# Optimization experiments

Hardware: AMD Instinct MI355X
Metric: run time of the kernel (lower is better)

Reference implementation:

```python
import jax, jax.numpy as jnp
import numpy as np

# 3x3 window roll offsets, row-major as in PatchShift2D.shift_content
SHIFTS = [(1, 1), (1, 0), (1, -1), (0, 1), (0, 0), (0, -1), (-1, 1), (-1, 0), (-1, -1)]
NUM_WIN = 9


def patch_shift(x, inv):
    # x: [B, T, H, W, C]; pad C up to multiple of 9 and H,W by 1, roll each
    # of the 9 channel groups by a distinct (h, w) offset, then crop back.
    B, T, H, W, C = x.shape
    Ch = int(np.ceil(C / NUM_WIN) * NUM_WIN)
    xp = jnp.pad(x, ((0, 0), (0, 0), (1, 1), (1, 1), (0, Ch - C)))
    m = -1 if inv else 1
    parts = jnp.split(xp, NUM_WIN, axis=-1)
    shifted = [jnp.roll(p, (m * sh, m * sw), axis=(2, 3))
               for p, (sh, sw) in zip(parts, SHIFTS)]
    return jnp.concatenate(shifted, axis=-1)[:, :, 1:H + 1, 1:W + 1, :C]


def _gelu(v):
    return jax.nn.gelu(v, approximate=False)  # torch nn.GELU default (erf)


def setup_inputs() -> dict:
    key = jax.random.key(0)
    ks = jax.random.split(key, 14)
    B, T, H, W, C = 2, 8, 56, 56, 512
    HID = 1024
    s = 0.02
    return {
        "x": jax.random.normal(ks[0], (B, T, H, W, C), dtype=jnp.float32),
        "fc_w": s * jax.random.normal(ks[1], (C, HID), dtype=jnp.float32),
        "fc_b": jnp.zeros((HID,), jnp.float32),
        "fc1_w": s * jax.random.normal(ks[2], (HID, C), dtype=jnp.float32),
        "fc1_b": jnp.zeros((C,), jnp.float32),
        "fc2_w": s * jax.random.normal(ks[3], (HID, C), dtype=jnp.float32),
        "fc2_b": jnp.zeros((C,), jnp.float32),
        "rw1_w": s * jax.random.normal(ks[4], (C, C // 4), dtype=jnp.float32),
        "rw1_b": jnp.zeros((C // 4,), jnp.float32),
        "rw2_w": s * jax.random.normal(ks[5], (C // 4, 2 * C), dtype=jnp.float32),
        "rw2_b": jnp.zeros((2 * C,), jnp.float32),
        "proj_w": s * jax.random.normal(ks[6], (C, C), dtype=jnp.float32),
        "proj_b": jnp.zeros((C,), jnp.float32),
    }


def reference(x, fc_w, fc_b, fc1_w, fc1_b, fc2_w, fc2_b,
              rw1_w, rw1_b, rw2_w, rw2_b, proj_w, proj_b):
    B, T, H, W, C = x.shape
    xh = _gelu(x @ fc_w + fc_b)                                  # [B,T,H,W,HID]
    h = patch_shift(_gelu(patch_shift(xh, False) @ fc1_w + fc1_b), True)  # [B,T,H,W,C]
    w = _gelu(xh @ fc2_w + fc2_b)                                 # [B,T,H,W,C]
    a = (h + w).mean(axis=(1, 2, 3))                              # [B,C]
    a = _gelu(a @ rw1_w + rw1_b) @ rw2_w + rw2_b                  # [B,2C]
    a = jax.nn.softmax(a.reshape(B, C, 2).transpose(2, 0, 1), axis=0)  # [2,B,C]
    a = a[:, :, None, None, None, :]                              # [2,B,1,1,1,C]
    out = h * a[0] + w * a[1]
    return out @ proj_w + proj_b
```

## Files before the change

### kernel.cpp

```cpp
#include <hip/hip_runtime.h>
#include <hip/hip_bf16.h>
#include <stdint.h>


typedef __attribute__((ext_vector_type(8))) short short8;
typedef __attribute__((ext_vector_type(4))) float floatx4;
typedef unsigned int uint;
typedef unsigned short ushort;

#define NTOK   50176
#define HWIMG  3136

__device__ __forceinline__ float gelu_exact(float v) {
    return 0.5f * v * (1.0f + erff(v * 0.70710678118654752440f));
}
__device__ __forceinline__ float gelu_fast(float v) {
    float u = v * (0.7978845608f + 0.0356774081f * v * v);
    return v * __builtin_amdgcn_rcpf(1.0f + __expf(-2.0f * u));
}

__device__ __forceinline__ int shift_h(int g) { return 1 - g / 3; }
__device__ __forceinline__ int shift_w(int g) { return 1 - g % 3; }

typedef const __attribute__((address_space(1))) uint* gas_ptr;
typedef __attribute__((address_space(3))) uint* las_ptr;

__device__ __forceinline__ void async_copy16(const void* g, void* l) {
    gas_ptr gp = (gas_ptr)(uintptr_t)g;
    las_ptr lp = (las_ptr)(uint32_t)(uintptr_t)l;
    __builtin_amdgcn_global_load_lds(gp, lp, 16, 0, 0);
}

template <int EPI>
__global__ __launch_bounds__(256) void gemm_bt(
    const __hip_bfloat16* __restrict__ A,
    const __hip_bfloat16* __restrict__ Bt,
    const float* __restrict__ bias,
    void* __restrict__ Cout, __hip_bfloat16* __restrict__ Cout2,
    float* __restrict__ ssum, int N, int K)
{
    __shared__ __hip_bfloat16 As[128 * 32];
    __shared__ __hip_bfloat16 Bs[128 * 32];

    const int t    = threadIdx.x;
    const int lane = t & 63;
    const int wave = t >> 6;
    const int wm   = wave >> 1;
    const int wn   = wave & 1;

    const int nbn  = gridDim.x;
    const int flat = blockIdx.y * nbn + blockIdx.x;
    const int xcd  = flat & 7;
    const int j    = flat >> 3;
    const int jd   = j / nbn;
    const int bm   = xcd * 49 + jd;
    const int bn   = j - jd * nbn;

    const __hip_bfloat16* ga0 = A  + (size_t)(bm * 128 + (t >> 2)) * K + (t & 3) * 8;
    const __hip_bfloat16* ga1 = ga0 + (size_t)64 * K;
    const __hip_bfloat16* gb0 = Bt + (size_t)(bn * 128 + (t >> 2)) * K + (t & 3) * 8;
    const __hip_bfloat16* gb1 = gb0 + (size_t)64 * K;
    __hip_bfloat16* la0 = &As[t * 8];
    __hip_bfloat16* la1 = &As[t * 8 + 2048];
    __hip_bfloat16* lb0 = &Bs[t * 8];
    __hip_bfloat16* lb1 = &Bs[t * 8 + 2048];

    floatx4 acc[4][4] = {};

    const int kq = (lane >> 4) * 8;
    const int ml = lane & 15;

    for (int k0 = 0; k0 < K; k0 += 32) {
        async_copy16(ga0, la0);
        async_copy16(ga1, la1);
        async_copy16(gb0, lb0);
        async_copy16(gb1, lb1);
        ga0 += 32; ga1 += 32; gb0 += 32; gb1 += 32;
        asm volatile("s_waitcnt vmcnt(0)" ::: "memory");
        __syncthreads();

        short8 af[4], bf[4];
#pragma unroll
        for (int i = 0; i < 4; i++) {
            af[i] = *(const short8*)&As[(wm * 64 + i * 16 + ml) * 32 + kq];
            bf[i] = *(const short8*)&Bs[(wn * 64 + i * 16 + ml) * 32 + kq];
        }
#pragma unroll
        for (int mi = 0; mi < 4; mi++)
#pragma unroll
            for (int ni = 0; ni < 4; ni++)
                acc[mi][ni] = __builtin_amdgcn_mfma_f32_16x16x32_bf16(
                    af[mi], bf[ni], acc[mi][ni], 0, 0, 0);
        __syncthreads();
    }

    const int rq = (lane >> 4) * 4;

    int cols[4], gsh[4], gsw[4];
    float bv[4];
    float sum[4] = {0.f, 0.f, 0.f, 0.f};
#pragma unroll
    for (int ni = 0; ni < 4; ni++) {
        const int col = bn * 128 + wn * 64 + ni * 16 + ml;
        cols[ni] = col;
        bv[ni] = bias[col];
        if (EPI == 1) { const int g = col / 114; gsh[ni] = shift_h(g); gsw[ni] = shift_w(g); }
        if (EPI == 2) { const int g = col / 57;  gsh[ni] = shift_h(g); gsw[ni] = shift_w(g); }
    }

#pragma unroll
    for (int mi = 0; mi < 4; mi++) {
        const int row0 = bm * 128 + wm * 64 + mi * 16 + rq;
        int phr[4], pwr[4];
        if (EPI == 1 || EPI == 2) {
            const int bt_ = row0 / HWIMG;
            const int rem = row0 - bt_ * HWIMG;
            const int ph0 = rem / 56;
            const int pw0 = rem - ph0 * 56;
#pragma unroll
            for (int r = 0; r < 4; r++) {
                int pw = pw0 + r, ph = ph0;
                if (pw >= 56) { pw -= 56; ph += 1; }
                if (ph >= 56) { ph = 0; }
                phr[r] = ph; pwr[r] = pw;
            }
        }
#pragma unroll
        for (int ni = 0; ni < 4; ni++) {
            const int col = cols[ni];
#pragma unroll
            for (int r = 0; r < 4; r++) {
                const int tok = row0 + r;
                float v = acc[mi][ni][r] + bv[ni];
                if (EPI != 0) v = gelu_fast(v);
                if (EPI == 0) {
                    ((float*)Cout)[(size_t)tok * N + col] = v;
                } else if (EPI == 1) {
                    const __hip_bfloat16 bvv = __float2bfloat16(v);
                    ((__hip_bfloat16*)Cout)[(size_t)tok * N + col] = bvv;
                    const int th = phr[r] + gsh[ni], tw = pwr[r] + gsw[ni];
                    if ((unsigned)th < 56u && (unsigned)tw < 56u)
                        Cout2[(size_t)(tok + gsh[ni] * 56 + gsw[ni]) * N + col] = bvv;
                } else if (EPI == 2) {
                    const int th = phr[r] - gsh[ni], tw = pwr[r] - gsw[ni];
                    if ((unsigned)th < 56u && (unsigned)tw < 56u) {
                        ((__hip_bfloat16*)Cout)[(size_t)(tok - gsh[ni] * 56 - gsw[ni]) * N + col]
                            = __float2bfloat16(v);
                        sum[ni] += v;
                    }
                } else {
                    ((__hip_bfloat16*)Cout)[(size_t)tok * N + col] = __float2bfloat16(v);
                    sum[ni] += v;
                }
            }
        }
    }

    if (EPI == 2 || EPI == 3) {
        const int b = (bm >= 196) ? 1 : 0;
#pragma unroll
        for (int ni = 0; ni < 4; ni++) {
            float s = sum[ni];
            s += __shfl_xor(s, 16, 64);
            s += __shfl_xor(s, 32, 64);
            if (lane < 16) atomicAdd(&ssum[b * 512 + cols[ni]], s);
        }
    }
}

template <int C, int GS, int SGN>
__global__ __launch_bounds__(256) void zero_holes(__hip_bfloat16* __restrict__ buf)
{
    const int i = blockIdx.x * 256 + threadIdx.x;
    const int c = i % C;
    const int p = i / C;
    const int bt = p / 220, fp = p % 220;
    int oh, ow;
    if (fp < 56)       { oh = 0;        ow = fp; }
    else if (fp < 112) { oh = 55;       ow = fp - 56; }
    else if (fp < 166) { oh = fp - 111; ow = 0; }
    else               { oh = fp - 165; ow = 55; }
    const int g = c / GS;
    const int ih = oh - SGN * shift_h(g);
    const int iw = ow - SGN * shift_w(g);
    if ((unsigned)ih >= 56u || (unsigned)iw >= 56u)
        buf[((size_t)(bt * HWIMG + oh * 56 + ow)) * C + c] = __float2bfloat16(0.0f);
}

__global__ __launch_bounds__(256) void cvt_x(const float4* __restrict__ x,
                                             __hip_bfloat16* __restrict__ xb)
{
    int i = blockIdx.x * 256 + threadIdx.x;
    float4 v = x[i];
    __hip_bfloat16 b0 = __float2bfloat16(v.x);
    __hip_bfloat16 b1 = __float2bfloat16(v.y);
    __hip_bfloat16 b2 = __float2bfloat16(v.z);
    __hip_bfloat16 b3 = __float2bfloat16(v.w);
    uint2 o;
    o.x = (uint)*(ushort*)&b0 | ((uint)*(ushort*)&b1 << 16);
    o.y = (uint)*(ushort*)&b2 | ((uint)*(ushort*)&b3 << 16);
    *(uint2*)&xb[(size_t)i * 4] = o;
}

__global__ __launch_bounds__(256) void prep_w(
    const float* __restrict__ fcw,  const float* __restrict__ fc1w,
    const float* __restrict__ fc2w, const float* __restrict__ projw,
    __hip_bfloat16* __restrict__ fcwT, __hip_bfloat16* __restrict__ fc1T,
    __hip_bfloat16* __restrict__ fc2T, __hip_bfloat16* __restrict__ projT)
{
    int i = blockIdx.x * 256 + threadIdx.x;
    if (i < 524288) {
        int n = i >> 9, k = i & 511;
        fcwT[i] = __float2bfloat16(fcw[k * 1024 + n]);
    } else if (i < 1048576) {
        int j = i - 524288;
        int n = j >> 10, k = j & 1023;
        fc1T[j] = __float2bfloat16(fc1w[k * 512 + n]);
    } else if (i < 1572864) {
        int j = i - 1048576;
        int n = j >> 10, k = j & 1023;
        fc2T[j] = __float2bfloat16(fc2w[k * 512 + n]);
    } else if (i < 1835008) {
        int j = i - 1572864;
        int n = j >> 9, k = j & 511;
        projT[j] = __float2bfloat16(projw[k * 512 + n]);
    }
}

__global__ __launch_bounds__(256) void tiny_mlp(
    const float* __restrict__ s0, const float* __restrict__ s1,
    const float* __restrict__ rw1_w, const float* __restrict__ rw1_b,
    const float* __restrict__ rw2_w, const float* __restrict__ rw2_b,
    float* __restrict__ a0, float* __restrict__ a1)
{
    __shared__ float mean[1024];
    __shared__ float z[256];
    __shared__ float av[2048];
    const int t = threadIdx.x;
    for (int i = t; i < 1024; i += 256)
        mean[i] = (s0[i] + s1[i]) * (1.0f / 25088.0f);
    __syncthreads();
    {
        const int b = t >> 7, j = t & 127;
        float acc = rw1_b[j];
        for (int cc = 0; cc < 512; cc++)
            acc += mean[b * 512 + cc] * rw1_w[cc * 128 + j];
        z[t] = gelu_exact(acc);
    }
    __syncthreads();
    for (int i = t; i < 2048; i += 256) {
        const int b = i >> 10, o = i & 1023;
        float acc = rw2_b[o];
        for (int j = 0; j < 128; j++)
            acc += z[b * 128 + j] * rw2_w[j * 1024 + o];
        av[i] = acc;
    }
    __syncthreads();
    for (int i = t; i < 1024; i += 256) {
        const int b = i >> 9, cc = i & 511;
        const float x0 = av[b * 1024 + 2 * cc];
        const float x1 = av[b * 1024 + 2 * cc + 1];
        const float m = fmaxf(x0, x1);
        const float e0 = expf(x0 - m), e1 = expf(x1 - m);
        const float inv = 1.0f / (e0 + e1);
        a0[i] = e0 * inv;
        a1[i] = e1 * inv;
    }
}

__device__ __forceinline__ float bf_lo(uint u) { return __uint_as_float(u << 16); }
__device__ __forceinline__ float bf_hi(uint u) { return __uint_as_float(u & 0xffff0000u); }
__device__ __forceinline__ uint pack_bf2(float lo, float hi) {
    __hip_bfloat16 a = __float2bfloat16(lo), b = __float2bfloat16(hi);
    return (uint)*(ushort*)&a | ((uint)*(ushort*)&b << 16);
}

__global__ __launch_bounds__(256) void combine(
    const uint4* __restrict__ hs4, const uint4* __restrict__ w4,
    const float* __restrict__ a0, const float* __restrict__ a1,
    uint4* __restrict__ hw4)
{
    const int i = blockIdx.x * 256 + threadIdx.x;
    const int ck = i & 63;
    const int tok = i >> 6;
    const int b = (tok >= 25088) ? 1 : 0;
    const float4* A0 = (const float4*)&a0[b * 512 + ck * 8];
    const float4* A1 = (const float4*)&a1[b * 512 + ck * 8];
    const float4 s0l = A0[0], s0h = A0[1];
    const float4 s1l = A1[0], s1h = A1[1];
    const uint4 h = hs4[i], w = w4[i];
    uint4 o;
    o.x = pack_bf2(bf_lo(h.x) * s0l.x + bf_lo(w.x) * s1l.x,
                   bf_hi(h.x) * s0l.y + bf_hi(w.x) * s1l.y);
    o.y = pack_bf2(bf_lo(h.y) * s0l.z + bf_lo(w.y) * s1l.z,
                   bf_hi(h.y) * s0l.w + bf_hi(w.y) * s1l.w);
    o.z = pack_bf2(bf_lo(h.z) * s0h.x + bf_lo(w.z) * s1h.x,
                   bf_hi(h.z) * s0h.y + bf_hi(w.z) * s1h.y);
    o.w = pack_bf2(bf_lo(h.w) * s0h.z + bf_lo(w.w) * s1h.z,
                   bf_hi(h.w) * s0h.w + bf_hi(w.w) * s1h.w);
    hw4[i] = o;
}

extern "C" void kernel_launch(void* const* d_in, const int* in_sizes, int n_in,
                              void* d_out, int out_size, void* d_ws, size_t ws_size,
                              hipStream_t stream)
{
    const float* x      = (const float*)d_in[0];
    const float* fc_w   = (const float*)d_in[1];
    const float* fc_b   = (const float*)d_in[2];
    const float* fc1_w  = (const float*)d_in[3];
    const float* fc1_b  = (const float*)d_in[4];
    const float* fc2_w  = (const float*)d_in[5];
    const float* fc2_b  = (const float*)d_in[6];
    const float* rw1_w  = (const float*)d_in[7];
    const float* rw1_b  = (const float*)d_in[8];
    const float* rw2_w  = (const float*)d_in[9];
    const float* rw2_b  = (const float*)d_in[10];
    const float* proj_w = (const float*)d_in[11];
    const float* proj_b = (const float*)d_in[12];

    uint8_t* ws = (uint8_t*)d_ws;
    __hip_bfloat16* xh  = (__hip_bfloat16*)(ws);
    __hip_bfloat16* xb  = (__hip_bfloat16*)(ws + 102760448);
    uint8_t* wt         = ws + 102760448 + 51380224;
    __hip_bfloat16* fcwT  = (__hip_bfloat16*)(wt);
    __hip_bfloat16* fc1T  = fcwT + 524288;
    __hip_bfloat16* fc2T  = fc1T + 524288;
    __hip_bfloat16* projT = fc2T + 524288;
    float* s0 = (float*)(wt + 3670016);
    float* s1 = s0 + 1024;
    float* a0 = s1 + 1024;
    float* a1 = a0 + 1024;

    __hip_bfloat16* xs   = (__hip_bfloat16*)d_out;
    __hip_bfloat16* wbuf = (__hip_bfloat16*)d_out;
    __hip_bfloat16* hs   = xb;
    __hip_bfloat16* hw   = xh;

    hipMemsetAsync(s0, 0, 8192, stream);

    zero_holes<1024, 114, +1><<<14080, 256, 0, stream>>>(xs);
    cvt_x<<<25088, 256, 0, stream>>>((const float4*)x, xb);
    prep_w<<<7168, 256, 0, stream>>>(fc_w, fc1_w, fc2_w, proj_w, fcwT, fc1T, fc2T, projT);

    gemm_bt<1><<<dim3(8, 392), 256, 0, stream>>>(xb, fcwT, fc_b, xh, xs, nullptr, 1024, 512);
    zero_holes<512, 57, -1><<<7040, 256, 0, stream>>>(hs);
    gemm_bt<2><<<dim3(4, 392), 256, 0, stream>>>(xs, fc1T, fc1_b, hs, nullptr, s0, 512, 1024);
    gemm_bt<3><<<dim3(4, 392), 256, 0, stream>>>(xh, fc2T, fc2_b, wbuf, nullptr, s1, 512, 1024);
    tiny_mlp<<<1, 256, 0, stream>>>(s0, s1, rw1_w, rw1_b, rw2_w, rw2_b, a0, a1);
    combine<<<12544, 256, 0, stream>>>((const uint4*)hs, (const uint4*)wbuf, a0, a1, (uint4*)hw);
    gemm_bt<0><<<dim3(4, 392), 256, 0, stream>>>(hw, projT, proj_b, d_out, nullptr, nullptr, 512, 512);
}
```

Baseline: 663.4 us.

## Double-buffer GEMM LDS tiles and transpose MFMA output for vectorized epilogue stores

```diff
diff --git a/kernel.cpp b/kernel.cpp
--- a/kernel.cpp
+++ b/kernel.cpp
@@ -21,6 +21,11 @@
 
 __device__ __forceinline__ int shift_h(int g) { return 1 - g / 3; }
 __device__ __forceinline__ int shift_w(int g) { return 1 - g % 3; }
+
+__device__ __forceinline__ uint pack_bf2(float lo, float hi) {
+    __hip_bfloat16 a = __float2bfloat16(lo), b = __float2bfloat16(hi);
+    return (uint)*(ushort*)&a | ((uint)*(ushort*)&b << 16);
+}
 
 typedef const __attribute__((address_space(1))) uint* gas_ptr;
 typedef __attribute__((address_space(3))) uint* las_ptr;
@@ -39,8 +44,8 @@
     void* __restrict__ Cout, __hip_bfloat16* __restrict__ Cout2,
     float* __restrict__ ssum, int N, int K)
 {
-    __shared__ __hip_bfloat16 As[128 * 32];
-    __shared__ __hip_bfloat16 Bs[128 * 32];
+    __shared__ __align__(16) __hip_bfloat16 As[2][128 * 32];
+    __shared__ __align__(16) __hip_bfloat16 Bs[2][128 * 32];
 
     const int t    = threadIdx.x;
     const int lane = t & 63;
@@ -60,97 +65,134 @@
     const __hip_bfloat16* ga1 = ga0 + (size_t)64 * K;
     const __hip_bfloat16* gb0 = Bt + (size_t)(bn * 128 + (t >> 2)) * K + (t & 3) * 8;
     const __hip_bfloat16* gb1 = gb0 + (size_t)64 * K;
-    __hip_bfloat16* la0 = &As[t * 8];
-    __hip_bfloat16* la1 = &As[t * 8 + 2048];
-    __hip_bfloat16* lb0 = &Bs[t * 8];
-    __hip_bfloat16* lb1 = &Bs[t * 8 + 2048];
+    const int t8 = t * 8;
 
     floatx4 acc[4][4] = {};
-
     const int kq = (lane >> 4) * 8;
     const int ml = lane & 15;
 
-    for (int k0 = 0; k0 < K; k0 += 32) {
-        async_copy16(ga0, la0);
-        async_copy16(ga1, la1);
-        async_copy16(gb0, lb0);
-        async_copy16(gb1, lb1);
+    auto stage = [&](int buf) {
+        async_copy16(ga0, &As[buf][t8]);
+        async_copy16(ga1, &As[buf][t8 + 2048]);
+        async_copy16(gb0, &Bs[buf][t8]);
+        async_copy16(gb1, &Bs[buf][t8 + 2048]);
         ga0 += 32; ga1 += 32; gb0 += 32; gb1 += 32;
-        asm volatile("s_waitcnt vmcnt(0)" ::: "memory");
-        __syncthreads();
+    };
+
+    const int nt = K >> 5;
+    stage(0);
+    __syncthreads();
+
+    for (int tt = 0; tt < nt; ++tt) {
+        const int cur = tt & 1;
+        if (tt + 1 < nt) stage(cur ^ 1);
 
         short8 af[4], bf[4];
 #pragma unroll
         for (int i = 0; i < 4; i++) {
-            af[i] = *(const short8*)&As[(wm * 64 + i * 16 + ml) * 32 + kq];
-            bf[i] = *(const short8*)&Bs[(wn * 64 + i * 16 + ml) * 32 + kq];
+            af[i] = *(const short8*)&As[cur][(wm * 64 + i * 16 + ml) * 32 + kq];
+            bf[i] = *(const short8*)&Bs[cur][(wn * 64 + i * 16 + ml) * 32 + kq];
         }
 #pragma unroll
         for (int mi = 0; mi < 4; mi++)
 #pragma unroll
             for (int ni = 0; ni < 4; ni++)
                 acc[mi][ni] = __builtin_amdgcn_mfma_f32_16x16x32_bf16(
-                    af[mi], bf[ni], acc[mi][ni], 0, 0, 0);
+                    bf[ni], af[mi], acc[mi][ni], 0, 0, 0);
+
         __syncthreads();
     }
 
-    const int rq = (lane >> 4) * 4;
-
-    int cols[4], gsh[4], gsw[4];
-    float bv[4];
-    float sum[4] = {0.f, 0.f, 0.f, 0.f};
+    const int rq  = (lane >> 4) * 4;
+    const int chb = bn * 128 + wn * 64 + rq;
+    const int tkb = bm * 128 + wm * 64 + ml;
+
+    float s_ac[4][4];
+    if (EPI == 2 || EPI == 3)
+#pragma unroll
+        for (int ni = 0; ni < 4; ni++)
+#pragma unroll
+            for (int r = 0; r < 4; r++) s_ac[ni][r] = 0.f;
+
 #pragma unroll
     for (int ni = 0; ni < 4; ni++) {
-        const int col = bn * 128 + wn * 64 + ni * 16 + ml;
-        cols[ni] = col;
-        bv[ni] = bias[col];
-        if (EPI == 1) { const int g = col / 114; gsh[ni] = shift_h(g); gsw[ni] = shift_w(g); }
-        if (EPI == 2) { const int g = col / 57;  gsh[ni] = shift_h(g); gsw[ni] = shift_w(g); }
-    }
-
-#pragma unroll
-    for (int mi = 0; mi < 4; mi++) {
-        const int row0 = bm * 128 + wm * 64 + mi * 16 + rq;
-        int phr[4], pwr[4];
+        const int ch0 = chb + ni * 16;
+        const float4 b4 = *(const float4*)&bias[ch0];
+        int gsh = 0, gsw = 0;
+        bool guni = true;
         if (EPI == 1 || EPI == 2) {
-            const int bt_ = row0 / HWIMG;
-            const int rem = row0 - bt_ * HWIMG;
-            const int ph0 = rem / 56;
-            const int pw0 = rem - ph0 * 56;
-#pragma unroll
-            for (int r = 0; r < 4; r++) {
-                int pw = pw0 + r, ph = ph0;
-                if (pw >= 56) { pw -= 56; ph += 1; }
-                if (ph >= 56) { ph = 0; }
-                phr[r] = ph; pwr[r] = pw;
+            const int DIV = (EPI == 1) ? 114 : 57;
+            const int g0 = ch0 / DIV, g3 = (ch0 + 3) / DIV;
+            guni = (g0 == g3);
+            gsh = shift_h(g0); gsw = shift_w(g0);
+        }
+#pragma unroll
+        for (int mi = 0; mi < 4; mi++) {
+            const int tok = tkb + mi * 16;
+            float v[4];
+            v[0] = acc[mi][ni][0] + b4.x;
+            v[1] = acc[mi][ni][1] + b4.y;
+            v[2] = acc[mi][ni][2] + b4.z;
+            v[3] = acc[mi][ni][3] + b4.w;
+            if (EPI != 0) {
+#pragma unroll
+                for (int r = 0; r < 4; r++) v[r] = gelu_fast(v[r]);
             }
-        }
-#pragma unroll
-        for (int ni = 0; ni < 4; ni++) {
-            const int col = cols[ni];
-#pragma unroll
-            for (int r = 0; r < 4; r++) {
-                const int tok = row0 + r;
-                float v = acc[mi][ni][r] + bv[ni];
-                if (EPI != 0) v = gelu_fast(v);
-                if (EPI == 0) {
-                    ((float*)Cout)[(size_t)tok * N + col] = v;
-                } else if (EPI == 1) {
-                    const __hip_bfloat16 bvv = __float2bfloat16(v);
-                    ((__hip_bfloat16*)Cout)[(size_t)tok * N + col] = bvv;
-                    const int th = phr[r] + gsh[ni], tw = pwr[r] + gsw[ni];
-                    if ((unsigned)th < 56u && (unsigned)tw < 56u)
-                        Cout2[(size_t)(tok + gsh[ni] * 56 + gsw[ni]) * N + col] = bvv;
-                } else if (EPI == 2) {
-                    const int th = phr[r] - gsh[ni], tw = pwr[r] - gsw[ni];
-                    if ((unsigned)th < 56u && (unsigned)tw < 56u) {
-                        ((__hip_bfloat16*)Cout)[(size_t)(tok - gsh[ni] * 56 - gsw[ni]) * N + col]
-                            = __float2bfloat16(v);
-                        sum[ni] += v;
+
+            if (EPI == 0) {
+                float4 o; o.x = v[0]; o.y = v[1]; o.z = v[2]; o.w = v[3];
+                *(float4*)&((float*)Cout)[(size_t)tok * N + ch0] = o;
+            } else {
+                uint2 u;
+                u.x = pack_bf2(v[0], v[1]);
+                u.y = pack_bf2(v[2], v[3]);
+
+                if (EPI == 1 || EPI == 3)
+                    *(uint2*)&((__hip_bfloat16*)Cout)[(size_t)tok * N + ch0] = u;
+
+                if (EPI == 1 || EPI == 2) {
+                    const int rem = tok - (tok / HWIMG) * HWIMG;
+                    const int ph = rem / 56, pw = rem - ph * 56;
+                    if (EPI == 1) {
+                        if (guni) {
+                            if ((unsigned)(ph + gsh) < 56u && (unsigned)(pw + gsw) < 56u)
+                                *(uint2*)&Cout2[(size_t)(tok + gsh * 56 + gsw) * N + ch0] = u;
+                        } else {
+#pragma unroll
+                            for (int r = 0; r < 4; r++) {
+                                const int g = (ch0 + r) / 114;
+                                const int sh = shift_h(g), sw = shift_w(g);
+                                if ((unsigned)(ph + sh) < 56u && (unsigned)(pw + sw) < 56u)
+                                    Cout2[(size_t)(tok + sh * 56 + sw) * N + ch0 + r]
+                                        = __float2bfloat16(v[r]);
+                            }
+                        }
+                    } else {
+                        if (guni) {
+                            if ((unsigned)(ph - gsh) < 56u && (unsigned)(pw - gsw) < 56u) {
+                                *(uint2*)&((__hip_bfloat16*)Cout)
+                                    [(size_t)(tok - gsh * 56 - gsw) * N + ch0] = u;
+#pragma unroll
+                                for (int r = 0; r < 4; r++) s_ac[ni][r] += v[r];
+                            }
+                        } else {
+#pragma unroll
+                            for (int r = 0; r < 4; r++) {
+                                const int g = (ch0 + r) / 57;
+                                const int sh = shift_h(g), sw = shift_w(g);
+                                if ((unsigned)(ph - sh) < 56u && (unsigned)(pw - sw) < 56u) {
+                                    ((__hip_bfloat16*)Cout)
+                                        [(size_t)(tok - sh * 56 - sw) * N + ch0 + r]
+                                        = __float2bfloat16(v[r]);
+                                    s_ac[ni][r] += v[r];
+                                }
+                            }
+                        }
                     }
-                } else {
-                    ((__hip_bfloat16*)Cout)[(size_t)tok * N + col] = __float2bfloat16(v);
-                    sum[ni] += v;
+                }
+                if (EPI == 3) {
+#pragma unroll
+                    for (int r = 0; r < 4; r++) s_ac[ni][r] += v[r];
                 }
             }
         }
@@ -159,12 +201,16 @@
     if (EPI == 2 || EPI == 3) {
         const int b = (bm >= 196) ? 1 : 0;
 #pragma unroll
-        for (int ni = 0; ni < 4; ni++) {
-            float s = sum[ni];
-            s += __shfl_xor(s, 16, 64);
-            s += __shfl_xor(s, 32, 64);
-            if (lane < 16) atomicAdd(&ssum[b * 512 + cols[ni]], s);
-        }
+        for (int ni = 0; ni < 4; ni++)
+#pragma unroll
+            for (int r = 0; r < 4; r++) {
+                float s = s_ac[ni][r];
+                s += __shfl_xor(s, 1, 64);
+                s += __shfl_xor(s, 2, 64);
+                s += __shfl_xor(s, 4, 64);
+                s += __shfl_xor(s, 8, 64);
+                if (ml == 0) atomicAdd(&ssum[b * 512 + chb + ni * 16 + r], s);
+            }
     }
 }
 
@@ -270,10 +316,6 @@
 
 __device__ __forceinline__ float bf_lo(uint u) { return __uint_as_float(u << 16); }
 __device__ __forceinline__ float bf_hi(uint u) { return __uint_as_float(u & 0xffff0000u); }
-__device__ __forceinline__ uint pack_bf2(float lo, float hi) {
-    __hip_bfloat16 a = __float2bfloat16(lo), b = __float2bfloat16(hi);
-    return (uint)*(ushort*)&a | ((uint)*(ushort*)&b << 16);
-}
 
 __global__ __launch_bounds__(256) void combine(
     const uint4* __restrict__ hs4, const uint4* __restrict__ w4,
```

Measured after the change: 699.0 us. +5.4%, slower.

## Fuse forward patch shift into fc1 GEMM A-operand load

Applied to the files above, without the earlier changes.

```diff
diff --git a/kernel.cpp b/kernel.cpp
--- a/kernel.cpp
+++ b/kernel.cpp
@@ -31,16 +31,16 @@
     __builtin_amdgcn_global_load_lds(gp, lp, 16, 0, 0);
 }
 
-template <int EPI>
+template <int EPI, bool SHIFTA>
 __global__ __launch_bounds__(256) void gemm_bt(
     const __hip_bfloat16* __restrict__ A,
     const __hip_bfloat16* __restrict__ Bt,
     const float* __restrict__ bias,
-    void* __restrict__ Cout, __hip_bfloat16* __restrict__ Cout2,
+    void* __restrict__ Cout,
     float* __restrict__ ssum, int N, int K)
 {
-    __shared__ __hip_bfloat16 As[128 * 32];
-    __shared__ __hip_bfloat16 Bs[128 * 32];
+    __shared__ __align__(16) __hip_bfloat16 As[128 * 32];
+    __shared__ __align__(16) __hip_bfloat16 Bs[128 * 32];
 
     const int t    = threadIdx.x;
     const int lane = t & 63;
@@ -56,27 +56,76 @@
     const int bm   = xcd * 49 + jd;
     const int bn   = j - jd * nbn;
 
-    const __hip_bfloat16* ga0 = A  + (size_t)(bm * 128 + (t >> 2)) * K + (t & 3) * 8;
+    const int ar0 = bm * 128 + (t >> 2);
+    const int ar1 = ar0 + 64;
+    const int ac  = (t & 3) * 8;
+
+    const __hip_bfloat16* ga0 = A  + (size_t)ar0 * K + ac;
     const __hip_bfloat16* ga1 = ga0 + (size_t)64 * K;
-    const __hip_bfloat16* gb0 = Bt + (size_t)(bn * 128 + (t >> 2)) * K + (t & 3) * 8;
+    const __hip_bfloat16* gb0 = Bt + (size_t)(bn * 128 + (t >> 2)) * K + ac;
     const __hip_bfloat16* gb1 = gb0 + (size_t)64 * K;
     __hip_bfloat16* la0 = &As[t * 8];
     __hip_bfloat16* la1 = &As[t * 8 + 2048];
     __hip_bfloat16* lb0 = &Bs[t * 8];
     __hip_bfloat16* lb1 = &Bs[t * 8 + 2048];
 
+    int oh0 = 0, ow0 = 0, oh1 = 0, ow1 = 0;
+    if (SHIFTA) {
+        const int rem0 = ar0 % HWIMG, rem1 = ar1 % HWIMG;
+        oh0 = rem0 / 56; ow0 = rem0 - oh0 * 56;
+        oh1 = rem1 / 56; ow1 = rem1 - oh1 * 56;
+    }
+
     floatx4 acc[4][4] = {};
 
     const int kq = (lane >> 4) * 8;
     const int ml = lane & 15;
 
     for (int k0 = 0; k0 < K; k0 += 32) {
-        async_copy16(ga0, la0);
-        async_copy16(ga1, la1);
         async_copy16(gb0, lb0);
         async_copy16(gb1, lb1);
-        ga0 += 32; ga1 += 32; gb0 += 32; gb1 += 32;
+        gb0 += 32; gb1 += 32;
+
+        uint4 av0 = {0, 0, 0, 0}, av1 = {0, 0, 0, 0};
+        if (SHIFTA) {
+            const int c0 = k0 + ac;
+            const int g  = c0 / 114;
+            const int ge = (c0 + 7) / 114;
+            if (g == ge) {
+                const int sh = shift_h(g), sw = shift_w(g);
+                const int off = sh * 56 + sw;
+                if ((unsigned)(oh0 - sh) < 56u && (unsigned)(ow0 - sw) < 56u)
+                    av0 = *(const uint4*)(A + (size_t)(ar0 - off) * K + c0);
+                if ((unsigned)(oh1 - sh) < 56u && (unsigned)(ow1 - sw) < 56u)
+                    av1 = *(const uint4*)(A + (size_t)(ar1 - off) * K + c0);
+            } else {
+                union { ushort us[8]; uint4 v; } p0, p1;
+#pragma unroll
+                for (int e = 0; e < 8; e++) {
+                    const int c  = c0 + e;
+                    const int gg = c / 114;
+                    const int sh = shift_h(gg), sw = shift_w(gg);
+                    const int off = sh * 56 + sw;
+                    ushort v0 = 0, v1 = 0;
+                    if ((unsigned)(oh0 - sh) < 56u && (unsigned)(ow0 - sw) < 56u)
+                        v0 = *(const ushort*)(A + (size_t)(ar0 - off) * K + c);
+                    if ((unsigned)(oh1 - sh) < 56u && (unsigned)(ow1 - sw) < 56u)
+                        v1 = *(const ushort*)(A + (size_t)(ar1 - off) * K + c);
+                    p0.us[e] = v0; p1.us[e] = v1;
+                }
+                av0 = p0.v; av1 = p1.v;
+            }
+        } else {
+            async_copy16(ga0, la0);
+            async_copy16(ga1, la1);
+            ga0 += 32; ga1 += 32;
+        }
+
         asm volatile("s_waitcnt vmcnt(0)" ::: "memory");
+        if (SHIFTA) {
+            *(uint4*)la0 = av0;
+            *(uint4*)la1 = av1;
+        }
         __syncthreads();
 
         short8 af[4], bf[4];
@@ -104,15 +153,14 @@
         const int col = bn * 128 + wn * 64 + ni * 16 + ml;
         cols[ni] = col;
         bv[ni] = bias[col];
-        if (EPI == 1) { const int g = col / 114; gsh[ni] = shift_h(g); gsw[ni] = shift_w(g); }
-        if (EPI == 2) { const int g = col / 57;  gsh[ni] = shift_h(g); gsw[ni] = shift_w(g); }
+        if (EPI == 2) { const int g = col / 57; gsh[ni] = shift_h(g); gsw[ni] = shift_w(g); }
     }
 
 #pragma unroll
     for (int mi = 0; mi < 4; mi++) {
         const int row0 = bm * 128 + wm * 64 + mi * 16 + rq;
         int phr[4], pwr[4];
-        if (EPI == 1 || EPI == 2) {
+        if (EPI == 2) {
             const int bt_ = row0 / HWIMG;
             const int rem = row0 - bt_ * HWIMG;
             const int ph0 = rem / 56;
@@ -136,11 +184,7 @@
                 if (EPI == 0) {
                     ((float*)Cout)[(size_t)tok * N + col] = v;
                 } else if (EPI == 1) {
-                    const __hip_bfloat16 bvv = __float2bfloat16(v);
-                    ((__hip_bfloat16*)Cout)[(size_t)tok * N + col] = bvv;
-                    const int th = phr[r] + gsh[ni], tw = pwr[r] + gsw[ni];
-                    if ((unsigned)th < 56u && (unsigned)tw < 56u)
-                        Cout2[(size_t)(tok + gsh[ni] * 56 + gsw[ni]) * N + col] = bvv;
+                    ((__hip_bfloat16*)Cout)[(size_t)tok * N + col] = __float2bfloat16(v);
                 } else if (EPI == 2) {
                     const int th = phr[r] - gsh[ni], tw = pwr[r] - gsw[ni];
                     if ((unsigned)th < 56u && (unsigned)tw < 56u) {
@@ -332,22 +376,20 @@
     float* a0 = s1 + 1024;
     float* a1 = a0 + 1024;
 
-    __hip_bfloat16* xs   = (__hip_bfloat16*)d_out;
     __hip_bfloat16* wbuf = (__hip_bfloat16*)d_out;
     __hip_bfloat16* hs   = xb;
     __hip_bfloat16* hw   = xh;
 
     hipMemsetAsync(s0, 0, 8192, stream);
 
-    zero_holes<1024, 114, +1><<<14080, 256, 0, stream>>>(xs);
     cvt_x<<<25088, 256, 0, stream>>>((const float4*)x, xb);
     prep_w<<<7168, 256, 0, stream>>>(fc_w, fc1_w, fc2_w, proj_w, fcwT, fc1T, fc2T, projT);
 
-    gemm_bt<1><<<dim3(8, 392), 256, 0, stream>>>(xb, fcwT, fc_b, xh, xs, nullptr, 1024, 512);
+    gemm_bt<1, false><<<dim3(8, 392), 256, 0, stream>>>(xb, fcwT, fc_b, xh, nullptr, 1024, 512);
     zero_holes<512, 57, -1><<<7040, 256, 0, stream>>>(hs);
-    gemm_bt<2><<<dim3(4, 392), 256, 0, stream>>>(xs, fc1T, fc1_b, hs, nullptr, s0, 512, 1024);
-    gemm_bt<3><<<dim3(4, 392), 256, 0, stream>>>(xh, fc2T, fc2_b, wbuf, nullptr, s1, 512, 1024);
+    gemm_bt<2, true><<<dim3(4, 392), 256, 0, stream>>>(xh, fc1T, fc1_b, hs, s0, 512, 1024);
+    gemm_bt<3, false><<<dim3(4, 392), 256, 0, stream>>>(xh, fc2T, fc2_b, wbuf, s1, 512, 1024);
     tiny_mlp<<<1, 256, 0, stream>>>(s0, s1, rw1_w, rw1_b, rw2_w, rw2_b, a0, a1);
     combine<<<12544, 256, 0, stream>>>((const uint4*)hs, (const uint4*)wbuf, a0, a1, (uint4*)hw);
-    gemm_bt<0><<<dim3(4, 392), 256, 0, stream>>>(hw, projT, proj_b, d_out, nullptr, nullptr, 512, 512);
-}
+    gemm_bt<0, false><<<dim3(4, 392), 256, 0, stream>>>(hw, projT, proj_b, d_out, nullptr, 512, 512);
+}
```

Result: faster. 621.3 us (-6.3%).
